# Kernel optimization log

Measured on AMD Instinct MI355X. Metric: run time of the kernel, lower is better.

The kernel has to match this reference:

```python
import jax, jax.numpy as jnp
import numpy as np
from jax import lax

B, T, V, D, H, C = 256, 1024, 5000, 100, 64, 2


def setup_inputs() -> dict:
    key = jax.random.key(0)
    k0, k1, k2, k3, k4 = jax.random.split(key, 5)
    tokens = jax.random.randint(k0, (B, T), 0, V)  # 0 is the mask/pad id
    E = jax.random.normal(k1, (V, D), dtype=jnp.float32) * 0.05
    W = jax.random.normal(k2, (D, H), dtype=jnp.float32) * (1.0 / np.sqrt(D))
    U = jax.random.normal(k3, (H, H), dtype=jnp.float32) * (1.0 / np.sqrt(H))
    b = jnp.zeros((H,), dtype=jnp.float32)
    Wd = jax.random.normal(k4, (H, C), dtype=jnp.float32) * (1.0 / np.sqrt(H))
    bd = jnp.zeros((C,), dtype=jnp.float32)
    return {"tokens": tokens, "E": E, "W": W, "U": U, "b": b, "Wd": Wd, "bd": bd}


def reference(tokens, E, W, U, b, Wd, bd):
    # Embedding with mask_zero=True: mask where token != 0
    x = E[tokens]                      # [B, T, D]
    mask = tokens != 0                 # [B, T] bool
    # Precompute input projection for all timesteps (batched GEMM).
    xW = jnp.einsum('btd,dh->bth', x, W) + b  # [B, T, H]

    def step(h, inp):
        xw_t, m_t = inp                # xw_t: [B,H], m_t: [B]
        h_new = jnp.tanh(xw_t + h @ U)
        # Keras masked recurrence: masked steps carry previous state/output.
        h = jnp.where(m_t[:, None], h_new, h)
        return h, h

    h0 = jnp.zeros((tokens.shape[0], U.shape[0]), dtype=xW.dtype)
    _, hs = lax.scan(step, h0, (jnp.swapaxes(xW, 0, 1), mask.T))  # hs: [T, B, H]
    hs = jnp.swapaxes(hs, 0, 1)        # [B, T, H]
    pooled = jnp.mean(hs, axis=1)      # tf.reduce_mean over time (unmasked mean)
    # Dropout is identity at inference.
    logits = pooled @ Wd + bd
    return jax.nn.sigmoid(logits)
```

## Files before the change

### kernel.cpp

```cpp
#include <hip/hip_runtime.h>

#define B_ 256
#define T_ 1024
#define V_ 5000
#define D_ 100
#define H_ 64
#define C_ 2

__global__ __launch_bounds__(256) void ew_kernel(const float* __restrict__ E,
                                                 const float* __restrict__ W,
                                                 const float* __restrict__ bias,
                                                 float* __restrict__ EW) {
    int idx = blockIdx.x * 256 + threadIdx.x;
    if (idx >= V_ * H_) return;
    int h = idx & (H_ - 1);
    int v = idx >> 6;
    float acc = bias[h];
    const float* Erow = E + v * D_;
    #pragma unroll 4
    for (int d = 0; d < D_; ++d) {
        acc = fmaf(Erow[d], W[d * H_ + h], acc);
    }
    EW[idx] = acc;
}

__device__ __forceinline__ float readlane_f(float v, int lane) {
    return __uint_as_float(__builtin_amdgcn_readlane(__float_as_uint(v), lane));
}

__global__ __launch_bounds__(64, 1) void rnn_kernel(const int* __restrict__ tokens,
                                                    const float* __restrict__ EW,
                                                    const float* __restrict__ U,
                                                    const float* __restrict__ Wd,
                                                    const float* __restrict__ bd,
                                                    float* __restrict__ out) {
    const int b = blockIdx.x;
    const int j = threadIdx.x;

    __shared__ int sh_tok[T_ + 2];

    float u[H_];
    #pragma unroll
    for (int k = 0; k < H_; ++k) {
        u[k] = U[k * H_ + j];
    }
    #pragma unroll
    for (int k = 0; k < H_; ++k) {
        asm volatile("" : "+v"(u[k]));
    }

    const int* tok = tokens + b * T_;
    #pragma unroll
    for (int k = 0; k < T_ / H_; ++k) {
        sh_tok[k * H_ + j] = tok[k * H_ + j];
    }
    if (j < 2) sh_tok[T_ + j] = 0;
    __syncthreads();

    float h = 0.f;
    float pooled = 0.f;

    int2 tkA = *(const int2*)&sh_tok[0];
    float xw0 = EW[tkA.x * H_ + j];
    float xw1 = EW[tkA.y * H_ + j];

    #define RNN_STEP(tokv, xwv)                                          \
    {                                                                    \
        float a0 = 0.f, a1 = 0.f, a2 = 0.f, a3 = 0.f;                    \
        _Pragma("unroll")                                                \
        for (int c = 0; c < 16; ++c) {                                   \
            a0 = fmaf(readlane_f(h, 4 * c + 0), u[4 * c + 0], a0);       \
            a1 = fmaf(readlane_f(h, 4 * c + 1), u[4 * c + 1], a1);       \
            a2 = fmaf(readlane_f(h, 4 * c + 2), u[4 * c + 2], a2);       \
            a3 = fmaf(readlane_f(h, 4 * c + 3), u[4 * c + 3], a3);       \
        }                                                                \
        float x = ((a0 + a1) + (a2 + a3)) + (xwv);                       \
        float e = __expf(2.f * x);                                       \
        float r = __builtin_amdgcn_rcpf(e + 1.f);                        \
        float hn = fmaf(-2.f, r, 1.f);                                   \
        h = ((tokv) != 0) ? hn : h;                                      \
        pooled += h;                                                     \
    }

    for (int t = 0; t < T_; t += 2) {
        int2 tkB = *(const int2*)&sh_tok[t + 2];
        float xw2 = EW[tkB.x * H_ + j];
        float xw3 = EW[tkB.y * H_ + j];

        RNN_STEP(tkA.x, xw0);
        RNN_STEP(tkA.y, xw1);

        tkA = tkB;
        xw0 = xw2;
        xw1 = xw3;
    }
    #undef RNN_STEP

    float p = pooled * (1.0f / (float)T_);
    float v0 = p * Wd[j * C_ + 0];
    float v1 = p * Wd[j * C_ + 1];
    #pragma unroll
    for (int off = 32; off >= 1; off >>= 1) {
        v0 += __shfl_down(v0, off, 64);
        v1 += __shfl_down(v1, off, 64);
    }
    if (j == 0) {
        float l0 = v0 + bd[0];
        float l1 = v1 + bd[1];
        out[b * C_ + 0] = 1.f / (1.f + __expf(-l0));
        out[b * C_ + 1] = 1.f / (1.f + __expf(-l1));
    }
}

extern "C" void kernel_launch(void* const* d_in, const int* in_sizes, int n_in,
                              void* d_out, int out_size, void* d_ws, size_t ws_size,
                              hipStream_t stream) {
    const int*   tokens = (const int*)  d_in[0];
    const float* E      = (const float*)d_in[1];
    const float* W      = (const float*)d_in[2];
    const float* U      = (const float*)d_in[3];
    const float* bias   = (const float*)d_in[4];
    const float* Wd     = (const float*)d_in[5];
    const float* bd     = (const float*)d_in[6];
    float* out = (float*)d_out;
    float* EW  = (float*)d_ws;

    ew_kernel<<<(V_ * H_ + 255) / 256, 256, 0, stream>>>(E, W, bias, EW);
    rnn_kernel<<<B_, H_, 0, stream>>>(tokens, EW, U, Wd, bd, out);
}
```

Baseline: 347.0 us.

## Split recurrent matvec across four waves with LDS reduction per step

Each batch row now runs on four wavefronts, and each wave computes a 16-wide slice of the h@U dot product using readlane broadcasts. The partial sums are combined through shared memory behind a barrier on every timestep. The tanh scale factor (2*log2e) is folded into EW and U so the kernel can use a raw exp2. The aim is to shorten the serial per-step dependency chain, at the cost of two LDS round trips and a workgroup barrier per step.

New measurement: 373.7 us. 7.7% more time.

```diff
diff --git a/kernel.cpp b/kernel.cpp
--- a/kernel.cpp
+++ b/kernel.cpp
@@ -6,6 +6,10 @@
 #define D_ 100
 #define H_ 64
 #define C_ 2
+
+typedef float f32x4 __attribute__((ext_vector_type(4)));
+
+#define SCALE_ 2.885390081777927f
 
 __global__ __launch_bounds__(256) void ew_kernel(const float* __restrict__ E,
                                                  const float* __restrict__ W,
@@ -21,94 +25,131 @@
     for (int d = 0; d < D_; ++d) {
         acc = fmaf(Erow[d], W[d * H_ + h], acc);
     }
-    EW[idx] = acc;
+    EW[idx] = SCALE_ * acc;
 }
 
 __device__ __forceinline__ float readlane_f(float v, int lane) {
     return __uint_as_float(__builtin_amdgcn_readlane(__float_as_uint(v), lane));
 }
 
-__global__ __launch_bounds__(64, 1) void rnn_kernel(const int* __restrict__ tokens,
-                                                    const float* __restrict__ EW,
-                                                    const float* __restrict__ U,
-                                                    const float* __restrict__ Wd,
-                                                    const float* __restrict__ bd,
-                                                    float* __restrict__ out) {
-    const int b = blockIdx.x;
-    const int j = threadIdx.x;
+__global__ __launch_bounds__(256, 1) void rnn_kernel(const int* __restrict__ tokens,
+                                                     const float* __restrict__ EW,
+                                                     const float* __restrict__ U,
+                                                     const float* __restrict__ Wd,
+                                                     const float* __restrict__ bd,
+                                                     float* __restrict__ out) {
+    const int b   = blockIdx.x;
+    const int tid = threadIdx.x;
+    const int w   = tid >> 6;
+    const int j   = tid & 63;
+    const int kbase = w << 4;
 
-    __shared__ int sh_tok[T_ + 2];
+    __shared__ int   sh_tok[T_ + 2];
+    __shared__ float sh_p[2][4][H_];
 
-    float u[H_];
+    f32x4 uq[4];
     #pragma unroll
-    for (int k = 0; k < H_; ++k) {
-        u[k] = U[k * H_ + j];
+    for (int c = 0; c < 4; ++c) {
+        #pragma unroll
+        for (int i = 0; i < 4; ++i) {
+            uq[c][i] = SCALE_ * U[(kbase + 4 * c + i) * H_ + j];
+        }
     }
-    #pragma unroll
-    for (int k = 0; k < H_; ++k) {
-        asm volatile("" : "+v"(u[k]));
-    }
+    asm volatile("" : "+v"(uq[0]), "+v"(uq[1]), "+v"(uq[2]), "+v"(uq[3]));
 
     const int* tok = tokens + b * T_;
     #pragma unroll
-    for (int k = 0; k < T_ / H_; ++k) {
-        sh_tok[k * H_ + j] = tok[k * H_ + j];
+    for (int k = 0; k < T_ / 256; ++k) {
+        sh_tok[k * 256 + tid] = tok[k * 256 + tid];
     }
-    if (j < 2) sh_tok[T_ + j] = 0;
+    if (tid < 2) sh_tok[T_ + tid] = 0;
     __syncthreads();
 
     float h = 0.f;
     float pooled = 0.f;
 
     int2 tkA = *(const int2*)&sh_tok[0];
-    float xw0 = EW[tkA.x * H_ + j];
-    float xw1 = EW[tkA.y * H_ + j];
+    float xw0 = 0.f, xw1 = 0.f;
+    if (w == 0) {
+        xw0 = EW[tkA.x * H_ + j];
+        xw1 = EW[tkA.y * H_ + j];
+    }
 
-    #define RNN_STEP(tokv, xwv)                                          \
+    #define RL_GROUP(g)                                                  \
     {                                                                    \
-        float a0 = 0.f, a1 = 0.f, a2 = 0.f, a3 = 0.f;                    \
-        _Pragma("unroll")                                                \
-        for (int c = 0; c < 16; ++c) {                                   \
-            a0 = fmaf(readlane_f(h, 4 * c + 0), u[4 * c + 0], a0);       \
-            a1 = fmaf(readlane_f(h, 4 * c + 1), u[4 * c + 1], a1);       \
-            a2 = fmaf(readlane_f(h, 4 * c + 2), u[4 * c + 2], a2);       \
-            a3 = fmaf(readlane_f(h, 4 * c + 3), u[4 * c + 3], a3);       \
-        }                                                                \
-        float x = ((a0 + a1) + (a2 + a3)) + (xwv);                       \
-        float e = __expf(2.f * x);                                       \
-        float r = __builtin_amdgcn_rcpf(e + 1.f);                        \
+        float s0 = readlane_f(h, kbase + 8 * (g) + 0);                   \
+        float s1 = readlane_f(h, kbase + 8 * (g) + 1);                   \
+        float s2 = readlane_f(h, kbase + 8 * (g) + 2);                   \
+        float s3 = readlane_f(h, kbase + 8 * (g) + 3);                   \
+        float s4 = readlane_f(h, kbase + 8 * (g) + 4);                   \
+        float s5 = readlane_f(h, kbase + 8 * (g) + 5);                   \
+        float s6 = readlane_f(h, kbase + 8 * (g) + 6);                   \
+        float s7 = readlane_f(h, kbase + 8 * (g) + 7);                   \
+        asm volatile("" : "+s"(s0), "+s"(s1), "+s"(s2), "+s"(s3),        \
+                          "+s"(s4), "+s"(s5), "+s"(s6), "+s"(s7));       \
+        a0 = fmaf(s0, uq[2 * (g) + 0][0], a0);                           \
+        a1 = fmaf(s1, uq[2 * (g) + 0][1], a1);                           \
+        a0 = fmaf(s2, uq[2 * (g) + 0][2], a0);                           \
+        a1 = fmaf(s3, uq[2 * (g) + 0][3], a1);                           \
+        a0 = fmaf(s4, uq[2 * (g) + 1][0], a0);                           \
+        a1 = fmaf(s5, uq[2 * (g) + 1][1], a1);                           \
+        a0 = fmaf(s6, uq[2 * (g) + 1][2], a0);                           \
+        a1 = fmaf(s7, uq[2 * (g) + 1][3], a1);                           \
+    }
+
+    #define RNN_STEP(par, tokv, xwv)                                     \
+    {                                                                    \
+        float a0 = (xwv), a1 = 0.f;                                      \
+        RL_GROUP(0) RL_GROUP(1)                                          \
+        sh_p[par][w][j] = a0 + a1;                                       \
+        asm volatile("s_waitcnt lgkmcnt(0)\n\ts_barrier" ::: "memory");  \
+        float p0 = sh_p[par][0][j];                                      \
+        float p1 = sh_p[par][1][j];                                      \
+        float p2 = sh_p[par][2][j];                                      \
+        float p3 = sh_p[par][3][j];                                      \
+        float x2 = (p0 + p1) + (p2 + p3);                                \
+        float ef = __builtin_amdgcn_exp2f(x2);                           \
+        float r  = __builtin_amdgcn_rcpf(ef + 1.f);                      \
         float hn = fmaf(-2.f, r, 1.f);                                   \
         h = ((tokv) != 0) ? hn : h;                                      \
         pooled += h;                                                     \
     }
 
     for (int t = 0; t < T_; t += 2) {
+        asm volatile("" :: "v"(uq[0]), "v"(uq[1]), "v"(uq[2]), "v"(uq[3]));
+
         int2 tkB = *(const int2*)&sh_tok[t + 2];
-        float xw2 = EW[tkB.x * H_ + j];
-        float xw3 = EW[tkB.y * H_ + j];
+        float xw2 = 0.f, xw3 = 0.f;
+        if (w == 0) {
+            xw2 = EW[tkB.x * H_ + j];
+            xw3 = EW[tkB.y * H_ + j];
+        }
 
-        RNN_STEP(tkA.x, xw0);
-        RNN_STEP(tkA.y, xw1);
+        RNN_STEP(0, tkA.x, xw0);
+        RNN_STEP(1, tkA.y, xw1);
 
         tkA = tkB;
         xw0 = xw2;
         xw1 = xw3;
     }
     #undef RNN_STEP
+    #undef RL_GROUP
 
-    float p = pooled * (1.0f / (float)T_);
-    float v0 = p * Wd[j * C_ + 0];
-    float v1 = p * Wd[j * C_ + 1];
-    #pragma unroll
-    for (int off = 32; off >= 1; off >>= 1) {
-        v0 += __shfl_down(v0, off, 64);
-        v1 += __shfl_down(v1, off, 64);
-    }
-    if (j == 0) {
-        float l0 = v0 + bd[0];
-        float l1 = v1 + bd[1];
-        out[b * C_ + 0] = 1.f / (1.f + __expf(-l0));
-        out[b * C_ + 1] = 1.f / (1.f + __expf(-l1));
+    if (tid < 64) {
+        float p = pooled * (1.0f / (float)T_);
+        float v0 = p * Wd[j * C_ + 0];
+        float v1 = p * Wd[j * C_ + 1];
+        #pragma unroll
+        for (int off = 32; off >= 1; off >>= 1) {
+            v0 += __shfl_down(v0, off, 64);
+            v1 += __shfl_down(v1, off, 64);
+        }
+        if (j == 0) {
+            float l0 = v0 + bd[0];
+            float l1 = v1 + bd[1];
+            out[b * C_ + 0] = 1.f / (1.f + __expf(-l0));
+            out[b * C_ + 1] = 1.f / (1.f + __expf(-l1));
+        }
     }
 }
 
@@ -126,5 +167,5 @@
     float* EW  = (float*)d_ws;
 
     ew_kernel<<<(V_ * H_ + 255) / 256, 256, 0, stream>>>(E, W, bias, EW);
-    rnn_kernel<<<B_, H_, 0, stream>>>(tokens, EW, U, Wd, bd, out);
+    rnn_kernel<<<B_, 256, 0, stream>>>(tokens, EW, U, Wd, bd, out);
 }
```

## Compute recurrent h@U with split-bf16 MFMA instead of readlane FMAs

Applied to the files above, without the earlier changes.

Replaces the per-step 64 readlane+FMA dot product with MFMA 16x16x32 bf16 operations, using a hi/lo bf16 split of both h and U (three products) to keep near-fp32 accuracy. h is exchanged through LDS each step, and the tanh scale factor is folded into EW and U so that exp2 can be used directly. This targets the serial recurrence latency. In exchange it adds an LDS round trip and a chain of 24 dependent MFMAs per step, and it drops the lo*lo term, which costs some precision.

Result: slower. 390.1 us (+12.4%).

```diff
diff --git a/kernel.cpp b/kernel.cpp
--- a/kernel.cpp
+++ b/kernel.cpp
@@ -6,6 +6,11 @@
 #define D_ 100
 #define H_ 64
 #define C_ 2
+
+typedef float f32x4v __attribute__((ext_vector_type(4)));
+typedef short bf16x8 __attribute__((ext_vector_type(8)));
+
+#define SCALE_ 2.885390081777927f
 
 __global__ __launch_bounds__(256) void ew_kernel(const float* __restrict__ E,
                                                  const float* __restrict__ W,
@@ -21,11 +26,7 @@
     for (int d = 0; d < D_; ++d) {
         acc = fmaf(Erow[d], W[d * H_ + h], acc);
     }
-    EW[idx] = acc;
-}
-
-__device__ __forceinline__ float readlane_f(float v, int lane) {
-    return __uint_as_float(__builtin_amdgcn_readlane(__float_as_uint(v), lane));
+    EW[idx] = SCALE_ * acc;
 }
 
 __global__ __launch_bounds__(64, 1) void rnn_kernel(const int* __restrict__ tokens,
@@ -36,18 +37,43 @@
                                                     float* __restrict__ out) {
     const int b = blockIdx.x;
     const int j = threadIdx.x;
+    const int g = j >> 4;
+    const int c = j & 15;
 
     __shared__ int sh_tok[T_ + 2];
-
-    float u[H_];
+    __shared__ alignas(8) unsigned short sh_hhi[H_];
+    __shared__ alignas(8) unsigned short sh_hlo[H_];
+
+    union BF { unsigned u[4]; bf16x8 v; };
+    BF bhi[4][2], blo[4][2];
     #pragma unroll
-    for (int k = 0; k < H_; ++k) {
-        u[k] = U[k * H_ + j];
-    }
-    #pragma unroll
-    for (int k = 0; k < H_; ++k) {
-        asm volatile("" : "+v"(u[k]));
-    }
+    for (int t = 0; t < 4; ++t) {
+        #pragma unroll
+        for (int s = 0; s < 2; ++s) {
+            #pragma unroll
+            for (int w = 0; w < 4; ++w) {
+                int k0 = 32 * s + 16 * (w >> 1) + 4 * g + 2 * (w & 1);
+                float u0 = SCALE_ * U[(k0 + 0) * H_ + 16 * t + c];
+                float u1 = SCALE_ * U[(k0 + 1) * H_ + 16 * t + c];
+                unsigned c0, c1, e0, e1;
+                asm("v_cvt_pk_bf16_f32 %0, %1, %2" : "=v"(c0) : "v"(u0), "v"(u0));
+                asm("v_cvt_pk_bf16_f32 %0, %1, %2" : "=v"(c1) : "v"(u1), "v"(u1));
+                c0 &= 0xffffu; c1 &= 0xffffu;
+                float d0 = u0 - __uint_as_float(c0 << 16);
+                float d1 = u1 - __uint_as_float(c1 << 16);
+                asm("v_cvt_pk_bf16_f32 %0, %1, %2" : "=v"(e0) : "v"(d0), "v"(d0));
+                asm("v_cvt_pk_bf16_f32 %0, %1, %2" : "=v"(e1) : "v"(d1), "v"(d1));
+                bhi[t][s].u[w] = c0 | (c1 << 16);
+                blo[t][s].u[w] = (e0 & 0xffffu) | (e1 << 16);
+            }
+        }
+    }
+    asm volatile("" : "+v"(bhi[0][0].v), "+v"(bhi[0][1].v), "+v"(bhi[1][0].v),
+                      "+v"(bhi[1][1].v), "+v"(bhi[2][0].v), "+v"(bhi[2][1].v),
+                      "+v"(bhi[3][0].v), "+v"(bhi[3][1].v));
+    asm volatile("" : "+v"(blo[0][0].v), "+v"(blo[0][1].v), "+v"(blo[1][0].v),
+                      "+v"(blo[1][1].v), "+v"(blo[2][0].v), "+v"(blo[2][1].v),
+                      "+v"(blo[3][0].v), "+v"(blo[3][1].v));
 
     const int* tok = tokens + b * T_;
     #pragma unroll
@@ -57,6 +83,9 @@
     if (j < 2) sh_tok[T_ + j] = 0;
     __syncthreads();
 
+    const uint2* hhi64 = (const uint2*)sh_hhi;
+    const uint2* hlo64 = (const uint2*)sh_hlo;
+
     float h = 0.f;
     float pooled = 0.f;
 
@@ -64,25 +93,74 @@
     float xw0 = EW[tkA.x * H_ + j];
     float xw1 = EW[tkA.y * H_ + j];
 
-    #define RNN_STEP(tokv, xwv)                                          \
-    {                                                                    \
-        float a0 = 0.f, a1 = 0.f, a2 = 0.f, a3 = 0.f;                    \
-        _Pragma("unroll")                                                \
-        for (int c = 0; c < 16; ++c) {                                   \
-            a0 = fmaf(readlane_f(h, 4 * c + 0), u[4 * c + 0], a0);       \
-            a1 = fmaf(readlane_f(h, 4 * c + 1), u[4 * c + 1], a1);       \
-            a2 = fmaf(readlane_f(h, 4 * c + 2), u[4 * c + 2], a2);       \
-            a3 = fmaf(readlane_f(h, 4 * c + 3), u[4 * c + 3], a3);       \
-        }                                                                \
-        float x = ((a0 + a1) + (a2 + a3)) + (xwv);                       \
-        float e = __expf(2.f * x);                                       \
-        float r = __builtin_amdgcn_rcpf(e + 1.f);                        \
-        float hn = fmaf(-2.f, r, 1.f);                                   \
-        h = ((tokv) != 0) ? hn : h;                                      \
-        pooled += h;                                                     \
+    #define MFMA_(a, bb, cc) __builtin_amdgcn_mfma_f32_16x16x32_bf16((a), (bb), (cc), 0, 0, 0)
+
+    #define RNN_STEP(tokv, xwv)                                               \
+    {                                                                         \
+        unsigned whi_, wlo_;                                                  \
+        asm("v_cvt_pk_bf16_f32 %0, %1, %2" : "=v"(whi_) : "v"(h), "v"(h));    \
+        float dlo_ = h - __uint_as_float(whi_ << 16);                         \
+        asm("v_cvt_pk_bf16_f32 %0, %1, %2" : "=v"(wlo_) : "v"(dlo_), "v"(dlo_)); \
+        sh_hhi[j] = (unsigned short)whi_;                                     \
+        sh_hlo[j] = (unsigned short)wlo_;                                     \
+        asm volatile("" ::: "memory");      \
+        uint2 h0_ = hhi64[g];      uint2 h1_ = hhi64[4 + g];                  \
+        uint2 h2_ = hhi64[8 + g];  uint2 h3_ = hhi64[12 + g];                 \
+        uint2 l0_ = hlo64[g];      uint2 l1_ = hlo64[4 + g];                  \
+        uint2 l2_ = hlo64[8 + g];  uint2 l3_ = hlo64[12 + g];                 \
+        BF ahi0_, ahi1_, alo0_, alo1_;                                        \
+        ahi0_.u[0] = h0_.x; ahi0_.u[1] = h0_.y;                               \
+        ahi0_.u[2] = h1_.x; ahi0_.u[3] = h1_.y;                               \
+        ahi1_.u[0] = h2_.x; ahi1_.u[1] = h2_.y;                               \
+        ahi1_.u[2] = h3_.x; ahi1_.u[3] = h3_.y;                               \
+        alo0_.u[0] = l0_.x; alo0_.u[1] = l0_.y;                               \
+        alo0_.u[2] = l1_.x; alo0_.u[3] = l1_.y;                               \
+        alo1_.u[0] = l2_.x; alo1_.u[1] = l2_.y;                               \
+        alo1_.u[2] = l3_.x; alo1_.u[3] = l3_.y;                               \
+        f32x4v z_ = {0.f, 0.f, 0.f, 0.f};                                     \
+        f32x4v a0_ = MFMA_(ahi0_.v, bhi[0][0].v, z_);                         \
+        f32x4v a1_ = MFMA_(ahi0_.v, bhi[1][0].v, z_);                         \
+        f32x4v a2_ = MFMA_(ahi0_.v, bhi[2][0].v, z_);                         \
+        f32x4v a3_ = MFMA_(ahi0_.v, bhi[3][0].v, z_);                         \
+        a0_ = MFMA_(ahi1_.v, bhi[0][1].v, a0_);                               \
+        a1_ = MFMA_(ahi1_.v, bhi[1][1].v, a1_);                               \
+        a2_ = MFMA_(ahi1_.v, bhi[2][1].v, a2_);                               \
+        a3_ = MFMA_(ahi1_.v, bhi[3][1].v, a3_);                               \
+        a0_ = MFMA_(alo0_.v, bhi[0][0].v, a0_);                               \
+        a1_ = MFMA_(alo0_.v, bhi[1][0].v, a1_);                               \
+        a2_ = MFMA_(alo0_.v, bhi[2][0].v, a2_);                               \
+        a3_ = MFMA_(alo0_.v, bhi[3][0].v, a3_);                               \
+        a0_ = MFMA_(alo1_.v, bhi[0][1].v, a0_);                               \
+        a1_ = MFMA_(alo1_.v, bhi[1][1].v, a1_);                               \
+        a2_ = MFMA_(alo1_.v, bhi[2][1].v, a2_);                               \
+        a3_ = MFMA_(alo1_.v, bhi[3][1].v, a3_);                               \
+        a0_ = MFMA_(ahi0_.v, blo[0][0].v, a0_);                               \
+        a1_ = MFMA_(ahi0_.v, blo[1][0].v, a1_);                               \
+        a2_ = MFMA_(ahi0_.v, blo[2][0].v, a2_);                               \
+        a3_ = MFMA_(ahi0_.v, blo[3][0].v, a3_);                               \
+        a0_ = MFMA_(ahi1_.v, blo[0][1].v, a0_);                               \
+        a1_ = MFMA_(ahi1_.v, blo[1][1].v, a1_);                               \
+        a2_ = MFMA_(ahi1_.v, blo[2][1].v, a2_);                               \
+        a3_ = MFMA_(ahi1_.v, blo[3][1].v, a3_);                               \
+        float ya_ = (j & 16) ? a1_[0] : a0_[0];                               \
+        float yb_ = (j & 16) ? a3_[0] : a2_[0];                               \
+        float y_  = (j & 32) ? yb_ : ya_;                                     \
+        float x2_ = y_ + (xwv);                                               \
+        float ef_ = __builtin_amdgcn_exp2f(x2_);                              \
+        float r_  = __builtin_amdgcn_rcpf(ef_ + 1.f);                         \
+        float hn_ = fmaf(-2.f, r_, 1.f);                                      \
+        h = ((tokv) != 0) ? hn_ : h;                                          \
+        pooled += h;                                                          \
     }
 
     for (int t = 0; t < T_; t += 2) {
+        asm volatile("" :: "v"(bhi[0][0].v), "v"(bhi[0][1].v), "v"(bhi[1][0].v),
+                           "v"(bhi[1][1].v), "v"(bhi[2][0].v), "v"(bhi[2][1].v),
+                           "v"(bhi[3][0].v), "v"(bhi[3][1].v));
+        asm volatile("" :: "v"(blo[0][0].v), "v"(blo[0][1].v), "v"(blo[1][0].v),
+                           "v"(blo[1][1].v), "v"(blo[2][0].v), "v"(blo[2][1].v),
+                           "v"(blo[3][0].v), "v"(blo[3][1].v));
+
         int2 tkB = *(const int2*)&sh_tok[t + 2];
         float xw2 = EW[tkB.x * H_ + j];
         float xw3 = EW[tkB.y * H_ + j];
@@ -95,6 +173,7 @@
         xw1 = xw3;
     }
     #undef RNN_STEP
+    #undef MFMA_
 
     float p = pooled * (1.0f / (float)T_);
     float v0 = p * Wd[j * C_ + 0];
```
